# Performance work log

Measured on AMD Instinct MI355X. Metric: run time of the kernel, lower is better.

Reference implementation:

```python
import jax, jax.numpy as jnp
from jax import lax
import numpy as np

NC = 80      # classes
NM = 32      # mask coefficients
N = 8400     # anchors/boxes
H = 640; W = 640          # output canvas (img_shape)
MH = 160; MW = 160        # prototype mask resolution (img/4)
K = 100                   # max detections after NMS (fixed for jit)
CONF = 0.4
IOU_T = 0.7


def setup_inputs() -> dict:
    key = jax.random.key(0)
    k1, k2, k3, k4, k5, k6 = jax.random.split(key, 6)
    # well-formed boxes x1,y1,x2,y2 in pixel coords
    x1 = jax.random.uniform(k1, (1, 1, N), minval=0.0, maxval=float(W - 120))
    y1 = jax.random.uniform(k2, (1, 1, N), minval=0.0, maxval=float(H - 120))
    wh = jax.random.uniform(k3, (1, 2, N), minval=16.0, maxval=112.0)
    boxes = jnp.concatenate([x1, y1, x1 + wh[:, 0:1], y1 + wh[:, 1:2]], axis=1)
    cls = jax.random.uniform(k4, (1, NC, N), minval=0.0, maxval=0.6)  # some exceed CONF
    coeffs = jax.random.normal(k5, (1, NM, N)) * 0.5
    detect = jnp.concatenate([boxes, cls, coeffs], axis=1)   # [1, 4+NC+NM, N]
    segment = jax.random.normal(k6, (1, NM, MH, MW))
    return {"detect": detect, "segment": segment}


def _per_image(d, proto):
    mi = 4 + NC
    d = d.T                              # [N, 4+NC+NM]
    boxes = d[:, :4]                     # x1,y1,x2,y2
    cls = d[:, 4:mi]
    scores = jnp.max(cls, axis=1)
    cids = jnp.argmax(cls, axis=1)
    coeffs = d[:, mi:]                   # [N, NM]
    valid = scores >= CONF
    # sort by confidence descending (invalid last)
    order = jnp.argsort(jnp.where(valid, -scores, jnp.inf))
    b = boxes[order]; s = scores[order]; v = valid[order]
    c = cids[order]; co = coeffs[order]
    idx = jnp.arange(N)
    area = (b[:, 2] - b[:, 0]) * (b[:, 3] - b[:, 1])
    # greedy class-agnostic NMS (sequential over sorted boxes, vectorized inner)
    def nms_step(keep, i):
        bi = b[i]
        ix1 = jnp.maximum(bi[0], b[:, 0]); iy1 = jnp.maximum(bi[1], b[:, 1])
        ix2 = jnp.minimum(bi[2], b[:, 2]); iy2 = jnp.minimum(bi[3], b[:, 3])
        inter = jnp.maximum(ix2 - ix1, 0.0) * jnp.maximum(iy2 - iy1, 0.0)
        iou = inter / (area[i] + area - inter)
        sup = (iou >= IOU_T) & (idx > i) & keep[i]
        return keep & ~sup, None
    keep, _ = lax.scan(nms_step, v, idx)
    # mask-coefficient matmul for ALL boxes (as in source: masks @ segment_reshaped)
    mlog = co @ proto.reshape(NM, -1)    # [N, MH*MW]
    kept_scores = jnp.where(keep, s, -1.0)
    topv, topi = lax.top_k(kept_scores, K)   # first K survivors (already score-sorted)
    valid_k = topv >= CONF
    bk = b[topi]; ck = c[topi]
    prob = jax.nn.sigmoid(mlog[topi].reshape(K, MH, MW))
    hard = (prob > 0.5).astype(prob.dtype)               # binarize at mask res
    up = jax.image.resize(hard, (K, H, W), method="bilinear")  # upsample to canvas
    maskk = up > 0.0
    ysg = jnp.arange(H)[:, None]; xsg = jnp.arange(W)[None, :]
    onehot = jax.nn.one_hot(ck, NC, dtype=jnp.float32)   # [K, NC]
    bi = bk.astype(jnp.int32)
    # paint objects in descending-score order; each box region is overwritten
    def paint(canvas, inp):
        box, m, oh, vv = inp
        inbox = (xsg >= box[0]) & (xsg < box[2]) & (ysg >= box[1]) & (ysg < box[3]) & vv
        canvas = jnp.where(inbox[..., None],
                           jnp.where((m & inbox)[..., None], oh, 0.0),
                           canvas)
        return canvas, None
    canvas0 = jnp.zeros((H, W, NC), dtype=jnp.float32)
    canvas, _ = lax.scan(paint, canvas0, (bi, maskk, onehot, valid_k))
    return canvas


def reference(detect, segment):
    return jax.vmap(_per_image)(detect, segment)   # [B, H, W, NC]
```

## Files before the change

### kernel.cpp

```cpp
#include <hip/hip_runtime.h>

#define NCLS 80
#define NMK  32
#define NB   8400
#define MH_  160
#define MP   25600
#define IH   640
#define IW   640
#define KTOP 100
#define CONFT 0.4f
#define IOUT 0.7f
#define T_PRE 384
#define TW   (T_PRE/64)

__global__ __launch_bounds__(256) void k_prep(const float* __restrict__ det,
    float* __restrict__ key, int* __restrict__ cid, int* __restrict__ rank)
{
  int n = blockIdx.x*256 + threadIdx.x;
  if (n >= NB) return;
  float best = det[4*NB + n];
  int bc = 0;
  #pragma unroll 8
  for (int c = 1; c < NCLS; ++c){
    float v = det[(4+c)*NB + n];
    if (v > best){ best = v; bc = c; }
  }
  cid[n] = bc;
  key[n] = (best >= CONFT) ? -best : __builtin_inff();
  rank[n] = 0;
}

__global__ __launch_bounds__(256) void k_rank(const float* __restrict__ key, int* __restrict__ rank)
{
  __shared__ float tk[256];
  int n = blockIdx.x*256 + threadIdx.x;
  float kn = (n < NB) ? key[n] : 0.f;
  int j0 = blockIdx.y * 263;
  int j1 = min(j0 + 263, NB);
  int part = 0;
  for (int t0 = j0; t0 < j1; t0 += 256){
    int j = t0 + threadIdx.x;
    tk[threadIdx.x] = (j < NB) ? key[j] : 0.f;
    __syncthreads();
    int lim = min(256, j1 - t0);
    for (int jj = 0; jj < lim; ++jj){
      float kj = tk[jj];
      int jg = t0 + jj;
      part += ((kj < kn) || (kj == kn && jg < n)) ? 1 : 0;
    }
    __syncthreads();
  }
  if (n < NB && part) atomicAdd(&rank[n], part);
}

__global__ __launch_bounds__(256) void k_scatter(const float* __restrict__ det,
    const int* __restrict__ cid, const int* __restrict__ rank,
    int* __restrict__ perm, int* __restrict__ scid, float4* __restrict__ sbox)
{
  int n = blockIdx.x*256 + threadIdx.x;
  if (n >= NB) return;
  int r = rank[n];
  perm[r] = n;
  scid[r] = cid[n];
  float4 b;
  b.x = det[0*NB + n]; b.y = det[1*NB + n];
  b.z = det[2*NB + n]; b.w = det[3*NB + n];
  sbox[r] = b;
}

__global__ __launch_bounds__(1024) void k_nms2(const float* __restrict__ key,
    const float4* __restrict__ sbox, const int* __restrict__ scid, const int* __restrict__ perm,
    int* __restrict__ selorig, int4* __restrict__ selbox, int* __restrict__ selcid,
    int* __restrict__ nsel)
{
  __shared__ __align__(16) unsigned long long lsup[T_PRE*TW];
  __shared__ int keptpos[KTOP];
  __shared__ int s_nv;
  __shared__ int s_found;
  const int tid  = threadIdx.x;
  const int lane = tid & 63;
  const int wv   = tid >> 6;
  if (tid == 0) s_nv = 0;
  __syncthreads();
  {
    int cnt = 0;
    for (int n = tid; n < NB; n += 1024){
      unsigned long long bal = __ballot(key[n] < 1e38f);
      if (lane == 0) cnt += (int)__popcll(bal);
    }
    if (lane == 0 && cnt) atomicAdd(&s_nv, cnt);
  }
  for (int t = wv; t < TW*TW; t += 16){
    const int ti = t / TW, tj = t % TW;
    float4 bj = sbox[tj*64 + lane];
    float aj = (bj.z - bj.x) * (bj.w - bj.y);
    float4 bi_all = sbox[ti*64 + lane];
    float ai_all  = (bi_all.z - bi_all.x) * (bi_all.w - bi_all.y);
    const int jg = tj*64 + lane;
    unsigned long long myrow = 0ull;
    #pragma unroll 4
    for (int ii = 0; ii < 64; ++ii){
      float bix = __shfl(bi_all.x, ii, 64);
      float biy = __shfl(bi_all.y, ii, 64);
      float biz = __shfl(bi_all.z, ii, 64);
      float biw = __shfl(bi_all.w, ii, 64);
      float ai  = __shfl(ai_all,  ii, 64);
      float ix1 = fmaxf(bix, bj.x), iy1 = fmaxf(biy, bj.y);
      float ix2 = fminf(biz, bj.z), iy2 = fminf(biw, bj.w);
      float inter = fmaxf(ix2 - ix1, 0.f) * fmaxf(iy2 - iy1, 0.f);
      bool sup = (jg > ti*64 + ii) && (inter / (ai + aj - inter) >= IOUT);
      unsigned long long bal = __ballot(sup);
      if (lane == ii) myrow = bal;
    }
    lsup[(ti*64 + lane)*TW + tj] = myrow;
  }
  __syncthreads();

  if (wv == 0){
    const int nv = s_nv;
    unsigned long long keepw = 0ull;
    if (lane < TW){
      int nbits = nv - lane*64;
      if (nbits >= 64) keepw = ~0ull;
      else if (nbits > 0) keepw = (1ull << nbits) - 1ull;
    }
    int found = 0;
    const int lim = min(nv, T_PRE);
    unsigned long long r0 = (lane < TW) ? lsup[0*TW + lane] : 0ull;
    unsigned long long r1 = (lane < TW) ? lsup[1*TW + lane] : 0ull;
    for (int cand = 0; cand < lim; ++cand){
      unsigned long long r2 = (lane < TW && cand + 2 < T_PRE) ? lsup[(cand+2)*TW + lane] : 0ull;
      bool mine = (lane == (cand >> 6)) && ((keepw >> (cand & 63)) & 1ull);
      if (__ballot(mine)){
        if (lane == 0) keptpos[found] = cand;
        found++;
        if (found >= KTOP) break;
        keepw &= ~r0;
      }
      r0 = r1; r1 = r2;
    }
    if (found < KTOP && nv > T_PRE){
      float4 kbA = make_float4(0.f,0.f,0.f,0.f);
      float4 kbB = make_float4(0.f,0.f,0.f,0.f);
      if (lane < found)      kbA = sbox[keptpos[lane]];
      if (lane + 64 < found) kbB = sbox[keptpos[lane + 64]];
      for (int j = T_PRE; j < nv && found < KTOP; ++j){
        float4 bj = sbox[j];
        float ajj = (bj.z - bj.x) * (bj.w - bj.y);
        bool s = false;
        if (lane < found){
          float ka = (kbA.z - kbA.x) * (kbA.w - kbA.y);
          float ix1 = fmaxf(kbA.x, bj.x), iy1 = fmaxf(kbA.y, bj.y);
          float ix2 = fminf(kbA.z, bj.z), iy2 = fminf(kbA.w, bj.w);
          float inter = fmaxf(ix2 - ix1, 0.f) * fmaxf(iy2 - iy1, 0.f);
          s = inter / (ka + ajj - inter) >= IOUT;
        }
        if (lane + 64 < found){
          float ka = (kbB.z - kbB.x) * (kbB.w - kbB.y);
          float ix1 = fmaxf(kbB.x, bj.x), iy1 = fmaxf(kbB.y, bj.y);
          float ix2 = fminf(kbB.z, bj.z), iy2 = fminf(kbB.w, bj.w);
          float inter = fmaxf(ix2 - ix1, 0.f) * fmaxf(iy2 - iy1, 0.f);
          s = s || (inter / (ka + ajj - inter) >= IOUT);
        }
        if (!__ballot(s)){
          if (lane == 0) keptpos[found] = j;
          if (found < 64){ if (lane == found) kbA = bj; }
          else           { if (lane == found - 64) kbB = bj; }
          found++;
        }
      }
    }
    if (lane == 0) s_found = found;
  }
  __syncthreads();
  const int ns = s_found;
  if (tid < ns){
    int si = keptpos[tid];
    float4 b = sbox[si];
    selorig[tid] = perm[si];
    selbox[tid]  = make_int4((int)b.x, (int)b.y, (int)b.z, (int)b.w);
    selcid[tid]  = scid[si];
  }
  if (tid == 0) *nsel = ns;
}

__global__ __launch_bounds__(256) void k_mask(const float* __restrict__ det, const float* __restrict__ proto,
    const int* __restrict__ selorig, const int* __restrict__ nsel, unsigned int* __restrict__ hb)
{
  const int p    = blockIdx.x*256 + threadIdx.x;
  const int lane = threadIdx.x & 63;
  const int wword = (blockIdx.x*256 + (threadIdx.x & ~63)) >> 5;
  float pr[NMK];
  #pragma unroll
  for (int m = 0; m < NMK; ++m) pr[m] = proto[m*MP + p];
  const int ns = *nsel;
  const int k0 = blockIdx.y * 25;
  for (int kk = 0; kk < 25; ++kk){
    int k = k0 + kk;
    if (k >= ns) break;
    int so = selorig[k];
    const float* cf = det + 84*NB + so;
    float acc = 0.f;
    #pragma unroll
    for (int m = 0; m < NMK; ++m) acc = fmaf(cf[(size_t)m*NB], pr[m], acc);
    unsigned long long bal = __ballot(acc > 0.f);
    if (lane == 0)  hb[k*800 + wword]     = (unsigned int)bal;
    if (lane == 32) hb[k*800 + wword + 1] = (unsigned int)(bal >> 32);
  }
}

__global__ __launch_bounds__(256) void k_paint(const int4* __restrict__ selbox, const int* __restrict__ selcid,
    const int* __restrict__ nsel, const unsigned int* __restrict__ hb, float* __restrict__ out)
{
  __shared__ int4  sbx[KTOP];
  __shared__ int   scd[KTOP];
  __shared__ short wcls[IW];
  __shared__ short clist[KTOP];
  __shared__ int   ccount;
  const int y = blockIdx.x;
  const int tid = threadIdx.x;
  const int ns = *nsel;
  if (tid < ns){ sbx[tid] = selbox[tid]; scd[tid] = selcid[tid]; }
  if (tid == 0) ccount = 0;
  __syncthreads();
  if (tid == 0){
    int m = 0;
    for (int k = 0; k < ns; ++k)
      if (y >= sbx[k].y && y < sbx[k].w) clist[m++] = (short)k;
    ccount = m;
  }
  __syncthreads();
  const int m = ccount;
  const int fyi = (y - 2) >> 2;
  const int ylo = max(fyi, 0), yhi = min(fyi + 1, MH_ - 1);
  for (int x = tid; x < IW; x += 256){
    int cls = -1;
    for (int ci = m - 1; ci >= 0; --ci){
      int k = clist[ci];
      int4 b = sbx[k];
      if (x >= b.x && x < b.z){
        int fx = (x - 2) >> 2;
        int xlo = max(fx, 0), xhi = min(fx + 1, MH_ - 1);
        bool on = false;
        for (int ry = ylo; ry <= yhi; ++ry)
          for (int rx = xlo; rx <= xhi; ++rx){
            int pp = ry*MH_ + rx;
            on = on || ((hb[k*800 + (pp >> 5)] >> (pp & 31)) & 1u);
          }
        cls = on ? scd[k] : -1;
        break;
      }
    }
    wcls[x] = (short)cls;
  }
  __syncthreads();
  float4* o4 = (float4*)(out + (size_t)y * (IW*NCLS));
  for (int it = 0; it < 50; ++it){
    int f4 = it*256 + tid;
    int x  = f4 / 20;
    int c  = (f4 % 20) * 4;
    int wc = wcls[x];
    float4 v;
    v.x = (wc == c    ) ? 1.f : 0.f;
    v.y = (wc == c + 1) ? 1.f : 0.f;
    v.z = (wc == c + 2) ? 1.f : 0.f;
    v.w = (wc == c + 3) ? 1.f : 0.f;
    o4[f4] = v;
  }
}

extern "C" void kernel_launch(void* const* d_in, const int* in_sizes, int n_in,
                              void* d_out, int out_size, void* d_ws, size_t ws_size,
                              hipStream_t stream)
{
  const float* det   = (const float*)d_in[0];
  const float* proto = (const float*)d_in[1];
  float* out = (float*)d_out;
  char* w = (char*)d_ws;
  float*  key     = (float*)(w + 0);
  int*    cid     = (int*)  (w + 33600);
  int*    rank    = (int*)  (w + 67200);
  int*    perm    = (int*)  (w + 100800);
  int*    scid    = (int*)  (w + 134400);
  float4* sbox    = (float4*)(w + 168000);
  int*    selorig = (int*)  (w + 302400);
  int4*   selbox  = (int4*) (w + 302800);
  int*    selcid  = (int*)  (w + 304400);
  int*    nsel    = (int*)  (w + 304800);
  unsigned int* hb = (unsigned int*)(w + 304816);

  hipLaunchKernelGGL(k_prep,    dim3(33),      dim3(256),  0, stream, det, key, cid, rank);
  hipLaunchKernelGGL(k_rank,    dim3(33, 32),  dim3(256),  0, stream, key, rank);
  hipLaunchKernelGGL(k_scatter, dim3(33),      dim3(256),  0, stream, det, cid, rank, perm, scid, sbox);
  hipLaunchKernelGGL(k_nms2,    dim3(1),       dim3(1024), 0, stream, key, sbox, scid, perm,
                     selorig, selbox, selcid, nsel);
  hipLaunchKernelGGL(k_mask,    dim3(100, 4),  dim3(256),  0, stream, det, proto, selorig, nsel, hb);
  hipLaunchKernelGGL(k_paint,   dim3(640),     dim3(256),  0, stream, selbox, selcid, nsel, hb, out);
}
```

Measured before the change: 262.5 us.

## Split NMS into parallel suppression-matrix kernel and greedy pass; fuse valid count

Moves the 6x6 tile IoU suppression-matrix computation out of the single-block NMS kernel into a separate 36-block kernel that writes to global memory. The greedy kernel copies the matrix into LDS. The valid-box count is now computed in k_prep via per-wave ballots instead of a rescan of all 8400 keys. The mask kernel's K-split goes from 4 groups of 25 to 10 groups of 10 to give more blocks. This adds one launch and a global round-trip of the matrix, in exchange for parallelising work that previously ran on one CU.

```diff
diff --git a/kernel.cpp b/kernel.cpp
--- a/kernel.cpp
+++ b/kernel.cpp
@@ -14,20 +14,27 @@
 #define TW   (T_PRE/64)
 
 __global__ __launch_bounds__(256) void k_prep(const float* __restrict__ det,
-    float* __restrict__ key, int* __restrict__ cid, int* __restrict__ rank)
+    float* __restrict__ key, int* __restrict__ cid, int* __restrict__ rank,
+    int* __restrict__ nvp)
 {
   int n = blockIdx.x*256 + threadIdx.x;
-  if (n >= NB) return;
-  float best = det[4*NB + n];
-  int bc = 0;
-  #pragma unroll 8
-  for (int c = 1; c < NCLS; ++c){
-    float v = det[(4+c)*NB + n];
-    if (v > best){ best = v; bc = c; }
-  }
-  cid[n] = bc;
-  key[n] = (best >= CONFT) ? -best : __builtin_inff();
-  rank[n] = 0;
+  bool valid = false;
+  if (n < NB){
+    float best = det[4*NB + n];
+    int bc = 0;
+    #pragma unroll 8
+    for (int c = 1; c < NCLS; ++c){
+      float v = det[(4+c)*NB + n];
+      if (v > best){ best = v; bc = c; }
+    }
+    cid[n] = bc;
+    valid = best >= CONFT;
+    key[n] = valid ? -best : __builtin_inff();
+    rank[n] = 0;
+  }
+  unsigned long long bal = __ballot(valid);
+  if ((threadIdx.x & 63) == 0)
+    nvp[blockIdx.x*4 + (threadIdx.x >> 6)] = (int)__popcll(bal);
 }
 
 __global__ __launch_bounds__(256) void k_rank(const float* __restrict__ key, int* __restrict__ rank)
@@ -68,55 +75,66 @@
   sbox[r] = b;
 }
 
-__global__ __launch_bounds__(1024) void k_nms2(const float* __restrict__ key,
-    const float4* __restrict__ sbox, const int* __restrict__ scid, const int* __restrict__ perm,
+__global__ __launch_bounds__(64) void k_supmat(const float4* __restrict__ sbox,
+    unsigned long long* __restrict__ supmat)
+{
+  const int lane = threadIdx.x;
+  const int ti = blockIdx.x;
+  const int tj = blockIdx.y;
+  float4 bj = sbox[tj*64 + lane];
+  float aj = (bj.z - bj.x) * (bj.w - bj.y);
+  float4 bi_all = sbox[ti*64 + lane];
+  float ai_all  = (bi_all.z - bi_all.x) * (bi_all.w - bi_all.y);
+  const int jg = tj*64 + lane;
+  unsigned long long myrow = 0ull;
+  #pragma unroll 4
+  for (int ii = 0; ii < 64; ++ii){
+    float bix = __shfl(bi_all.x, ii, 64);
+    float biy = __shfl(bi_all.y, ii, 64);
+    float biz = __shfl(bi_all.z, ii, 64);
+    float biw = __shfl(bi_all.w, ii, 64);
+    float ai  = __shfl(ai_all,  ii, 64);
+    float ix1 = fmaxf(bix, bj.x), iy1 = fmaxf(biy, bj.y);
+    float ix2 = fminf(biz, bj.z), iy2 = fminf(biw, bj.w);
+    float inter = fmaxf(ix2 - ix1, 0.f) * fmaxf(iy2 - iy1, 0.f);
+    bool sup = (jg > ti*64 + ii) && (inter / (ai + aj - inter) >= IOUT);
+    unsigned long long bal = __ballot(sup);
+    if (lane == ii) myrow = bal;
+  }
+  supmat[(size_t)(ti*64 + lane)*TW + tj] = myrow;
+}
+
+__global__ __launch_bounds__(1024) void k_greedy(const float4* __restrict__ sbox,
+    const int* __restrict__ scid, const int* __restrict__ perm,
+    const unsigned long long* __restrict__ supmat, const int* __restrict__ nvp,
     int* __restrict__ selorig, int4* __restrict__ selbox, int* __restrict__ selcid,
     int* __restrict__ nsel)
 {
   __shared__ __align__(16) unsigned long long lsup[T_PRE*TW];
   __shared__ int keptpos[KTOP];
+  __shared__ int partial[192];
   __shared__ int s_nv;
   __shared__ int s_found;
-  const int tid  = threadIdx.x;
-  const int lane = tid & 63;
-  const int wv   = tid >> 6;
-  if (tid == 0) s_nv = 0;
-  __syncthreads();
+  const int tid = threadIdx.x;
   {
-    int cnt = 0;
-    for (int n = tid; n < NB; n += 1024){
-      unsigned long long bal = __ballot(key[n] < 1e38f);
-      if (lane == 0) cnt += (int)__popcll(bal);
-    }
-    if (lane == 0 && cnt) atomicAdd(&s_nv, cnt);
-  }
-  for (int t = wv; t < TW*TW; t += 16){
-    const int ti = t / TW, tj = t % TW;
-    float4 bj = sbox[tj*64 + lane];
-    float aj = (bj.z - bj.x) * (bj.w - bj.y);
-    float4 bi_all = sbox[ti*64 + lane];
-    float ai_all  = (bi_all.z - bi_all.x) * (bi_all.w - bi_all.y);
-    const int jg = tj*64 + lane;
-    unsigned long long myrow = 0ull;
-    #pragma unroll 4
-    for (int ii = 0; ii < 64; ++ii){
-      float bix = __shfl(bi_all.x, ii, 64);
-      float biy = __shfl(bi_all.y, ii, 64);
-      float biz = __shfl(bi_all.z, ii, 64);
-      float biw = __shfl(bi_all.w, ii, 64);
-      float ai  = __shfl(ai_all,  ii, 64);
-      float ix1 = fmaxf(bix, bj.x), iy1 = fmaxf(biy, bj.y);
-      float ix2 = fminf(biz, bj.z), iy2 = fminf(biw, bj.w);
-      float inter = fmaxf(ix2 - ix1, 0.f) * fmaxf(iy2 - iy1, 0.f);
-      bool sup = (jg > ti*64 + ii) && (inter / (ai + aj - inter) >= IOUT);
-      unsigned long long bal = __ballot(sup);
-      if (lane == ii) myrow = bal;
-    }
-    lsup[(ti*64 + lane)*TW + tj] = myrow;
-  }
-  __syncthreads();
-
-  if (wv == 0){
+    const float4* g4 = (const float4*)supmat;
+    float4* l4 = (float4*)lsup;
+    for (int idx = tid; idx < (T_PRE*TW)/2; idx += 1024) l4[idx] = g4[idx];
+    partial[tid & 191] = 0;
+  }
+  __syncthreads();
+  if (tid < 132) partial[tid] = nvp[tid];
+  __syncthreads();
+  if (tid < 64){
+    int s = partial[tid] + partial[tid + 64] + ((tid + 128 < 192) ? partial[tid + 128] : 0);
+    #pragma unroll
+    for (int sh = 32; sh > 0; sh >>= 1) s += __shfl_xor(s, sh, 64);
+    if (tid == 0) s_nv = s;
+  }
+  __syncthreads();
+
+  if (tid < 64){
+    const int lane = tid;
     const int nv = s_nv;
     unsigned long long keepw = 0ull;
     if (lane < TW){
@@ -194,8 +212,8 @@
   #pragma unroll
   for (int m = 0; m < NMK; ++m) pr[m] = proto[m*MP + p];
   const int ns = *nsel;
-  const int k0 = blockIdx.y * 25;
-  for (int kk = 0; kk < 25; ++kk){
+  const int k0 = blockIdx.y * 10;
+  for (int kk = 0; kk < 10; ++kk){
     int k = k0 + kk;
     if (k >= ns) break;
     int so = selorig[k];
@@ -287,13 +305,16 @@
   int4*   selbox  = (int4*) (w + 302800);
   int*    selcid  = (int*)  (w + 304400);
   int*    nsel    = (int*)  (w + 304800);
-  unsigned int* hb = (unsigned int*)(w + 304816);
-
-  hipLaunchKernelGGL(k_prep,    dim3(33),      dim3(256),  0, stream, det, key, cid, rank);
+  int*    nvp     = (int*)  (w + 304832);
+  unsigned int* hb = (unsigned int*)(w + 305408);
+  unsigned long long* supmat = (unsigned long long*)(w + 625408);
+
+  hipLaunchKernelGGL(k_prep,    dim3(33),      dim3(256),  0, stream, det, key, cid, rank, nvp);
   hipLaunchKernelGGL(k_rank,    dim3(33, 32),  dim3(256),  0, stream, key, rank);
   hipLaunchKernelGGL(k_scatter, dim3(33),      dim3(256),  0, stream, det, cid, rank, perm, scid, sbox);
-  hipLaunchKernelGGL(k_nms2,    dim3(1),       dim3(1024), 0, stream, key, sbox, scid, perm,
+  hipLaunchKernelGGL(k_supmat,  dim3(TW, TW),  dim3(64),   0, stream, sbox, supmat);
+  hipLaunchKernelGGL(k_greedy,  dim3(1),       dim3(1024), 0, stream, sbox, scid, perm, supmat, nvp,
                      selorig, selbox, selcid, nsel);
-  hipLaunchKernelGGL(k_mask,    dim3(100, 4),  dim3(256),  0, stream, det, proto, selorig, nsel, hb);
+  hipLaunchKernelGGL(k_mask,    dim3(100, 10), dim3(256),  0, stream, det, proto, selorig, nsel, hb);
   hipLaunchKernelGGL(k_paint,   dim3(640),     dim3(256),  0, stream, selbox, selcid, nsel, hb, out);
 }
```

After: 220.7 us. 15.9% less time.
